# Performance work log

Measured on AMD Instinct MI355X. Metric: run time of the kernel, lower is better.

Reference implementation:

```python
import jax, jax.numpy as jnp
import numpy as np

N = 50000
E = 800000
IN_CH = 128
HID = 64
HEADS = 4
EPS = 1e-5
NEG_SLOPE = 0.2


def _gat_conv(x, src, dst, W, a_src, a_dst, b, heads, out_ch, concat):
    n = x.shape[0]
    h = (x @ W).reshape(n, heads, out_ch)                      # [N,H,C]
    alpha_src = jnp.sum(h * a_src, axis=-1)                    # [N,H]
    alpha_dst = jnp.sum(h * a_dst, axis=-1)                    # [N,H]
    e = jax.nn.leaky_relu(alpha_src[src] + alpha_dst[dst], NEG_SLOPE)  # [E',H]
    # segment softmax over incoming edges of each destination node
    m = jax.ops.segment_max(e, dst, num_segments=n)            # [N,H]
    e = jnp.exp(e - m[dst])
    denom = jax.ops.segment_sum(e, dst, num_segments=n)        # [N,H]
    alpha = e / denom[dst]                                     # [E',H]
    msg = h[src] * alpha[:, :, None]                           # [E',H,C]
    out = jax.ops.segment_sum(msg, dst, num_segments=n)        # [N,H,C]
    if concat:
        out = out.reshape(n, heads * out_ch)
    else:
        out = out.mean(axis=1)
    return out + b


def _bn_eval(x, gamma, beta, mean, var):
    return (x - mean) * (gamma / jnp.sqrt(var + EPS)) + beta


def setup_inputs() -> dict:
    key = jax.random.key(0)
    ks = jax.random.split(key, 24)
    s = 0.1
    x = jax.random.normal(ks[0], (N, IN_CH), dtype=jnp.float32)
    edge_index = jax.random.randint(ks[1], (2, E), 0, N, dtype=jnp.int32)
    d0, d1 = IN_CH, HID * HEADS
    inp = {
        'x': x, 'edge_index': edge_index,
        # layer 0: in_ch -> hidden, heads=4, concat
        'W0': jax.random.normal(ks[2], (d0, HEADS * HID), jnp.float32) * s,
        'as0': jax.random.normal(ks[3], (HEADS, HID), jnp.float32) * s,
        'ad0': jax.random.normal(ks[4], (HEADS, HID), jnp.float32) * s,
        'b0': jax.random.normal(ks[5], (HEADS * HID,), jnp.float32) * s,
        # layer 1: hidden*heads -> hidden, heads=4, concat
        'W1': jax.random.normal(ks[6], (d1, HEADS * HID), jnp.float32) * s,
        'as1': jax.random.normal(ks[7], (HEADS, HID), jnp.float32) * s,
        'ad1': jax.random.normal(ks[8], (HEADS, HID), jnp.float32) * s,
        'b1': jax.random.normal(ks[9], (HEADS * HID,), jnp.float32) * s,
        # layer 2: hidden*heads -> 1, heads=1, no concat
        'W2': jax.random.normal(ks[10], (d1, 1), jnp.float32) * s,
        'as2': jax.random.normal(ks[11], (1, 1), jnp.float32) * s,
        'ad2': jax.random.normal(ks[12], (1, 1), jnp.float32) * s,
        'b2': jax.random.normal(ks[13], (1,), jnp.float32) * s,
        # batchnorm (eval) params for the two hidden layers
        'g0': jnp.ones((d1,), jnp.float32),
        'be0': jnp.zeros((d1,), jnp.float32),
        'm0': jax.random.normal(ks[14], (d1,), jnp.float32) * s,
        'v0': jnp.ones((d1,), jnp.float32),
        'g1': jnp.ones((d1,), jnp.float32),
        'be1': jnp.zeros((d1,), jnp.float32),
        'm1': jax.random.normal(ks[15], (d1,), jnp.float32) * s,
        'v1': jnp.ones((d1,), jnp.float32),
    }
    return inp


def reference(x, edge_index, W0, as0, ad0, b0, W1, as1, ad1, b1,
              W2, as2, ad2, b2, g0, be0, m0, v0, g1, be1, m1, v1):
    n = x.shape[0]
    loops = jnp.arange(n, dtype=edge_index.dtype)
    src = jnp.concatenate([edge_index[0], loops])  # add self-loops (PyG default)
    dst = jnp.concatenate([edge_index[1], loops])

    # layer 0 (no residual: shapes differ)
    h = _gat_conv(x, src, dst, W0, as0, ad0, b0, HEADS, HID, True)
    h = jax.nn.elu(_bn_eval(h, g0, be0, m0, v0))

    # layer 1 (residual: shapes match)
    res = h
    h = _gat_conv(h, src, dst, W1, as1, ad1, b1, HEADS, HID, True)
    h = jax.nn.elu(_bn_eval(h, g1, be1, m1, v1)) + res

    # output layer: heads=1, concat=False -> [N,1]
    out = _gat_conv(h, src, dst, W2, as2, ad2, b2, 1, 1, False)
    return out.squeeze(-1)
```

## Files before the change

kernel.cpp:

```cpp
#include <hip/hip_runtime.h>
#include <math.h>

#define NEG_SLOPE 0.2f
#define BN_EPS 1e-5f

typedef __attribute__((ext_vector_type(8))) short bf16x8;
typedef __attribute__((ext_vector_type(4))) float f32x4;

static __device__ __forceinline__ unsigned short f2bf(float f){
    unsigned u = __float_as_uint(f);
    u += 0x7FFFu + ((u >> 16) & 1u);
    return (unsigned short)(u >> 16);
}
static __device__ __forceinline__ float bf2f(unsigned short v){
    return __uint_as_float((unsigned)v << 16);
}

static __device__ __forceinline__ void gload_lds16(const void* g, void* l){
    __builtin_amdgcn_global_load_lds(
        (const __attribute__((address_space(1))) void*)g,
        (__attribute__((address_space(3))) void*)l, 16, 0, 0);
}

static __device__ __forceinline__ void repack_one(const float* __restrict__ W,
    unsigned short* __restrict__ whi, unsigned short* __restrict__ wlo, int o)
{
    const int j = o & 7, ln = (o >> 3) & 63, ct = (o >> 9) & 15, kt = o >> 13;
    const int k = kt * 32 + 8 * (ln >> 4) + j;
    const int col = ct * 16 + (ln & 15);
    const float v = W[k * 256 + col];
    const unsigned short hb = f2bf(v);
    whi[o] = hb; wlo[o] = f2bf(v - bf2f(hb));
}

__global__ void prep_kernel(const float* __restrict__ W0,
    unsigned short* __restrict__ w0hi, unsigned short* __restrict__ w0lo,
    const float* __restrict__ W1,
    unsigned short* __restrict__ w1hi, unsigned short* __restrict__ w1lo,
    int* __restrict__ deg, int N)
{
    const int bid = blockIdx.x, t = threadIdx.x;
    if (bid < 128){
        repack_one(W0, w0hi, w0lo, bid * 256 + t);
    } else if (bid < 384){
        repack_one(W1, w1hi, w1lo, (bid - 128) * 256 + t);
    } else {
        const int i = (bid - 384) * 256 + t;
        if (i < N) deg[i] = 1;
    }
}

template<int K>
__global__ __launch_bounds__(256) void mfma_gemm_alpha(
    const float* __restrict__ x,
    const unsigned short* __restrict__ wbhi, const unsigned short* __restrict__ wblo,
    const float* __restrict__ a_s, const float* __restrict__ a_d,
    unsigned short* __restrict__ hout,
    float* __restrict__ asrc, float* __restrict__ adst, int N)
{
    __shared__ float xaf[4][2][64][4];
    __shared__ unsigned short wb[32][512];
    const int t = threadIdx.x, lane = t & 63, wid = t >> 6;
    const int n0 = blockIdx.x * 64;

    f32x4 acc[4][4];
#pragma unroll
    for (int rt = 0; rt < 4; ++rt)
#pragma unroll
        for (int q = 0; q < 4; ++q) acc[rt][q] = (f32x4){0.f, 0.f, 0.f, 0.f};

    for (int kt = 0; kt < K / 32; ++kt){
        __syncthreads();
#pragma unroll
        for (int ii = 0; ii < 2; ++ii){
            const int i = wid * 2 + ii;
            const int rt = i >> 1, half = i & 1;
            int node = n0 + rt * 16 + (lane & 15);
            if (node > N - 1) node = N - 1;
            const float* src = &x[(size_t)node * K + kt * 32 + 8 * (lane >> 4) + half * 4];
            gload_lds16(src, &xaf[rt][half][0][0]);
        }
#pragma unroll
        for (int ii = 0; ii < 8; ++ii){
            const int i = wid * 8 + ii;
            const int ct = i >> 1, plane = i & 1;
            const unsigned short* base = plane ? wblo : wbhi;
            gload_lds16(base + ((size_t)(kt * 16 + ct) * 64 + lane) * 8, &wb[i][0]);
        }
        __syncthreads();

        bf16x8 ahi[4], alo[4];
#pragma unroll
        for (int rt = 0; rt < 4; ++rt){
            const float4 f0 = *(const float4*)&xaf[rt][0][lane][0];
            const float4 f1 = *(const float4*)&xaf[rt][1][lane][0];
            const float fv[8] = {f0.x, f0.y, f0.z, f0.w, f1.x, f1.y, f1.z, f1.w};
#pragma unroll
            for (int j = 0; j < 8; ++j){
                const unsigned short hb = f2bf(fv[j]);
                ahi[rt][j] = (short)hb;
                alo[rt][j] = (short)f2bf(fv[j] - bf2f(hb));
            }
        }

#pragma unroll
        for (int q = 0; q < 4; ++q){
            const int cti = wid * 4 + q;
            const bf16x8 bhi = *(const bf16x8*)&wb[cti * 2 + 0][lane * 8];
            const bf16x8 blo = *(const bf16x8*)&wb[cti * 2 + 1][lane * 8];
#pragma unroll
            for (int rt = 0; rt < 4; ++rt){
                acc[rt][q] = __builtin_amdgcn_mfma_f32_16x16x32_bf16(ahi[rt], bhi, acc[rt][q], 0, 0, 0);
                acc[rt][q] = __builtin_amdgcn_mfma_f32_16x16x32_bf16(alo[rt], bhi, acc[rt][q], 0, 0, 0);
                acc[rt][q] = __builtin_amdgcn_mfma_f32_16x16x32_bf16(ahi[rt], blo, acc[rt][q], 0, 0, 0);
            }
        }
    }

    const int l15 = lane & 15, lg = lane >> 4;
    float avs[4], avd[4];
#pragma unroll
    for (int q = 0; q < 4; ++q){
        avs[q] = a_s[wid * 64 + q * 16 + l15];
        avd[q] = a_d[wid * 64 + q * 16 + l15];
    }
    float sp[4][4], dp[4][4];
#pragma unroll
    for (int rt = 0; rt < 4; ++rt){
#pragma unroll
        for (int reg = 0; reg < 4; ++reg){
            const int node = n0 + rt * 16 + lg * 4 + reg;
            float s = 0.f, d = 0.f;
            unsigned short hv[4];
#pragma unroll
            for (int q = 0; q < 4; ++q){
                const float v = acc[rt][q][reg];
                s = fmaf(v, avs[q], s); d = fmaf(v, avd[q], d);
                hv[q] = f2bf(v);
            }
            if (node < N){
#pragma unroll
                for (int q = 0; q < 4; ++q)
                    hout[(size_t)node * 256 + (wid * 4 + q) * 16 + l15] = hv[q];
            }
            sp[rt][reg] = s; dp[rt][reg] = d;
        }
    }
#pragma unroll
    for (int off = 1; off <= 8; off <<= 1){
#pragma unroll
        for (int rt = 0; rt < 4; ++rt)
#pragma unroll
            for (int reg = 0; reg < 4; ++reg){
                sp[rt][reg] += __shfl_xor(sp[rt][reg], off, 64);
                dp[rt][reg] += __shfl_xor(dp[rt][reg], off, 64);
            }
    }
    if (l15 == 0){
#pragma unroll
        for (int rt = 0; rt < 4; ++rt)
#pragma unroll
            for (int reg = 0; reg < 4; ++reg){
                const int node = n0 + rt * 16 + lg * 4 + reg;
                if (node < N){
                    asrc[(size_t)node * 4 + wid] = sp[rt][reg];
                    adst[(size_t)node * 4 + wid] = dp[rt][reg];
                }
            }
    }
}

__global__ void deg_hist_kernel(const int* __restrict__ ei, int E, int* __restrict__ deg){
    int e = blockIdx.x * blockDim.x + threadIdx.x;
    if (e < E) atomicAdd(&deg[ei[E + e]], 1);
}

__global__ __launch_bounds__(256) void part_sum_kernel(const int* __restrict__ deg,
                                                       int* __restrict__ bsum, int N)
{
    __shared__ int red[256];
    const int t = threadIdx.x;
    const int i0 = blockIdx.x * 1024 + t * 4;
    int s = 0;
    if (i0 + 3 < N){
        const int4 v = *(const int4*)&deg[i0];
        s = v.x + v.y + v.z + v.w;
    } else {
#pragma unroll
        for (int j = 0; j < 4; ++j) if (i0 + j < N) s += deg[i0 + j];
    }
    red[t] = s; __syncthreads();
    for (int off = 128; off >= 1; off >>= 1){
        if (t < off) red[t] += red[t + off];
        __syncthreads();
    }
    if (t == 0) bsum[blockIdx.x] = red[0];
}

__global__ __launch_bounds__(256) void scan_part_kernel(int* __restrict__ bsum, int nb,
                                                        int* __restrict__ row, int N)
{
    __shared__ int sh[256];
    const int t = threadIdx.x;
    const int v = (t < nb) ? bsum[t] : 0;
    sh[t] = v; __syncthreads();
    for (int off = 1; off < 256; off <<= 1){
        int u = (t >= off) ? sh[t - off] : 0;
        __syncthreads();
        sh[t] += u;
        __syncthreads();
    }
    if (t < nb) bsum[t] = sh[t] - v;
    if (t == nb - 1) row[N] = sh[t];
}

__global__ __launch_bounds__(256) void distribute_kernel(const int* __restrict__ deg,
    const int* __restrict__ bsum, int* __restrict__ row, int* __restrict__ cursor, int N)
{
    __shared__ int ts[256];
    const int t = threadIdx.x;
    const int i0 = blockIdx.x * 1024 + t * 4;
    int d[4]; int s = 0;
#pragma unroll
    for (int j = 0; j < 4; ++j){ d[j] = (i0 + j < N) ? deg[i0 + j] : 0; s += d[j]; }
    ts[t] = s; __syncthreads();
    for (int off = 1; off < 256; off <<= 1){
        int u = (t >= off) ? ts[t - off] : 0;
        __syncthreads();
        ts[t] += u;
        __syncthreads();
    }
    int base = bsum[blockIdx.x] + ts[t] - s;
#pragma unroll
    for (int j = 0; j < 4; ++j){
        if (i0 + j < N){ row[i0 + j] = base; cursor[i0 + j] = base; base += d[j]; }
    }
}

__global__ void scatter_kernel(const int* __restrict__ ei, int E, int N,
                               int* __restrict__ cursor, int* __restrict__ csr)
{
    int e = blockIdx.x * blockDim.x + threadIdx.x;
    if (e >= E + N) return;
    int s, d;
    if (e < E){ s = ei[e]; d = ei[E + e]; } else { s = d = e - E; }
    int pos = atomicAdd(&cursor[d], 1);
    csr[pos] = s;
}

#define DEG_CAP 128
template<bool LAST>
__global__ __launch_bounds__(256) void agg4_kernel(
    const int* __restrict__ row, const int* __restrict__ csr,
    const float* __restrict__ asrc, const float* __restrict__ adst,
    const unsigned short* __restrict__ h,
    const float* __restrict__ b, const float* __restrict__ g,
    const float* __restrict__ be, const float* __restrict__ mean,
    const float* __restrict__ var,
    const float* __restrict__ res,
    float* __restrict__ outp,
    const float* __restrict__ W2,
    int N)
{
    __shared__ float plds[4][DEG_CAP * 4];
    __shared__ int   slds[4][DEG_CAP];
    const int wid = threadIdx.x >> 6, lane = threadIdx.x & 63;
    const int node = blockIdx.x * 4 + wid;
    if (node >= N) return;
    const int beg = row[node], end = row[node + 1], deg = end - beg;
    const int degc = deg < DEG_CAP ? deg : DEG_CAP;
    const int head = lane >> 4;

    const float4 ad = *(const float4*)&adst[(size_t)node * 4];

    float d0 = 0.f, d1 = 0.f, d2 = 0.f, d3 = 0.f;
    for (int i = lane; i < deg; i += 64){
        const int s = csr[beg + i];
        const float4 as = *(const float4*)&asrc[(size_t)s * 4];
        float v0 = as.x + ad.x, v1 = as.y + ad.y, v2 = as.z + ad.z, v3 = as.w + ad.w;
        v0 = v0 > 0.f ? v0 : NEG_SLOPE * v0;
        v1 = v1 > 0.f ? v1 : NEG_SLOPE * v1;
        v2 = v2 > 0.f ? v2 : NEG_SLOPE * v2;
        v3 = v3 > 0.f ? v3 : NEG_SLOPE * v3;
        const float p0 = __expf(v0), p1 = __expf(v1);
        const float p2 = __expf(v2), p3 = __expf(v3);
        d0 += p0; d1 += p1; d2 += p2; d3 += p3;
        if (i < DEG_CAP){
            *(float4*)&plds[wid][i * 4] = make_float4(p0, p1, p2, p3);
            slds[wid][i] = s << 9;
        }
    }
    for (int off = 32; off >= 1; off >>= 1){
        d0 += __shfl_xor(d0, off, 64); d1 += __shfl_xor(d1, off, 64);
        d2 += __shfl_xor(d2, off, 64); d3 += __shfl_xor(d3, off, 64);
    }

    float a0 = 0.f, a1 = 0.f, a2 = 0.f, a3 = 0.f;
    {
        const char* hb = (const char*)h + lane * 8;
        const float* pb = &plds[wid][0];
        const int* sb = &slds[wid][0];
#define EDGE_BODY(slot)                                                        \
        {                                                                      \
            const float p_ = pb[(slot) * 4 + head];                            \
            const ushort4 hv_ = *(const ushort4*)(hb + sb[slot]);              \
            a0 = fmaf(p_, bf2f(hv_.x), a0); a1 = fmaf(p_, bf2f(hv_.y), a1);    \
            a2 = fmaf(p_, bf2f(hv_.z), a2); a3 = fmaf(p_, bf2f(hv_.w), a3);    \
        }
        int i = 0;
        for (; i + 2 <= degc; i += 2){
            EDGE_BODY(i);
            EDGE_BODY(i + 1);
        }
        for (; i < degc; ++i) EDGE_BODY(i);
#undef EDGE_BODY
    }

    for (int jj = beg + DEG_CAP; jj < end; ++jj){
        const int s = csr[jj];
        const float4 as = *(const float4*)&asrc[(size_t)s * 4];
        float e0 = as.x + ad.x, e1 = as.y + ad.y, e2 = as.z + ad.z, e3 = as.w + ad.w;
        float eh = (head == 0) ? e0 : (head == 1) ? e1 : (head == 2) ? e2 : e3;
        eh = eh > 0.f ? eh : NEG_SLOPE * eh;
        const float p = __expf(eh);
        const ushort4 hv = *(const ushort4*)&h[(size_t)s * 256 + lane * 4];
        a0 = fmaf(p, bf2f(hv.x), a0); a1 = fmaf(p, bf2f(hv.y), a1);
        a2 = fmaf(p, bf2f(hv.z), a2); a3 = fmaf(p, bf2f(hv.w), a3);
    }

    const int l15 = lane & 15;
    const float dsel = (head == 0) ? d0 : (head == 1) ? d1 : (head == 2) ? d2 : d3;
    const float rdi = 1.f / dsel;
    const int c0 = head * 64 + 4 * l15;
    const float4 bv  = *(const float4*)&b[c0];
    const float4 gv  = *(const float4*)&g[c0];
    const float4 bev = *(const float4*)&be[c0];
    const float4 mv  = *(const float4*)&mean[c0];
    const float4 vv4 = *(const float4*)&var[c0];
    const float ava[4]  = {a0, a1, a2, a3};
    const float bva[4]  = {bv.x, bv.y, bv.z, bv.w};
    const float gva[4]  = {gv.x, gv.y, gv.z, gv.w};
    const float beva[4] = {bev.x, bev.y, bev.z, bev.w};
    const float mva[4]  = {mv.x, mv.y, mv.z, mv.w};
    const float vva[4]  = {vv4.x, vv4.y, vv4.z, vv4.w};
    float rh[4] = {0.f, 0.f, 0.f, 0.f};
    if (LAST){
        const float4 rv = *(const float4*)&res[(size_t)node * 256 + c0];
        rh[0] = rv.x; rh[1] = rv.y; rh[2] = rv.z; rh[3] = rv.w;
    }
    float vvv[4];
#pragma unroll
    for (int j = 0; j < 4; ++j){
        float v = ava[j] * rdi + bva[j];
        v = (v - mva[j]) * (gva[j] * rsqrtf(vva[j] + BN_EPS)) + beva[j];
        v = v > 0.f ? v : (__expf(v) - 1.f);
        vvv[j] = v + rh[j];
    }
    if (!LAST){
        *(float4*)&outp[(size_t)node * 256 + c0] =
            make_float4(vvv[0], vvv[1], vvv[2], vvv[3]);
    } else {
        const float4 w2v = *(const float4*)&W2[c0];
        float part = vvv[0] * w2v.x + vvv[1] * w2v.y + vvv[2] * w2v.z + vvv[3] * w2v.w;
        for (int off = 32; off >= 1; off >>= 1) part += __shfl_xor(part, off, 64);
        if (lane == 0) outp[node] = part;
    }
}

__global__ void agg2_kernel(const int* __restrict__ row, const int* __restrict__ csr,
                            const float* __restrict__ h2,
                            const float* __restrict__ as2, const float* __restrict__ ad2,
                            const float* __restrict__ b2, float* __restrict__ out, int N)
{
    const int n = blockIdx.x * blockDim.x + threadIdx.x;
    if (n >= N) return;
    const float A_s = as2[0];
    const float hd  = h2[n] * ad2[0];
    const int beg = row[n], end = row[n + 1];
    float den = 0.f, acc = 0.f;
    for (int i = beg; i < end; ++i){
        const float hv = h2[csr[i]];
        float a = fmaf(A_s, hv, hd);
        a = a > 0.f ? a : NEG_SLOPE * a;
        const float p = __expf(a);
        den += p; acc = fmaf(p, hv, acc);
    }
    out[n] = acc / den + b2[0];
}

extern "C" void kernel_launch(void* const* d_in, const int* in_sizes, int n_in,
                              void* d_out, int out_size, void* d_ws, size_t ws_size,
                              hipStream_t stream)
{
    const float* x   = (const float*)d_in[0];
    const int*   ei  = (const int*)  d_in[1];
    const float* W0  = (const float*)d_in[2];
    const float* as0 = (const float*)d_in[3];
    const float* ad0 = (const float*)d_in[4];
    const float* b0  = (const float*)d_in[5];
    const float* W1  = (const float*)d_in[6];
    const float* as1 = (const float*)d_in[7];
    const float* ad1 = (const float*)d_in[8];
    const float* b1  = (const float*)d_in[9];
    const float* W2  = (const float*)d_in[10];
    const float* as2 = (const float*)d_in[11];
    const float* ad2 = (const float*)d_in[12];
    const float* b2  = (const float*)d_in[13];
    const float* g0  = (const float*)d_in[14];
    const float* be0 = (const float*)d_in[15];
    const float* m0  = (const float*)d_in[16];
    const float* v0  = (const float*)d_in[17];
    const float* g1  = (const float*)d_in[18];
    const float* be1 = (const float*)d_in[19];
    const float* m1  = (const float*)d_in[20];
    const float* v1  = (const float*)d_in[21];

    const int N = in_sizes[0] / 128;
    const int E = in_sizes[1] / 2;
    const int EN = E + N;

    char* w = (char*)d_ws;
    unsigned short* H  = (unsigned short*)w;  w += (size_t)N * 256 * 2;
    float*    P0     = (float*)w;   w += (size_t)N * 256 * 4;
    float*    asrc   = (float*)w;   w += (size_t)N * 4 * 4;
    float*    adst   = (float*)w;   w += (size_t)N * 4 * 4;
    int*      deg    = (int*)w;     w += (size_t)N * 4;
    int*      cursor = (int*)w;     w += (size_t)N * 4;
    int*      csr    = (int*)w;     w += (size_t)EN * 4;
    float*    h2     = (float*)w;   w += (size_t)N * 4;
    int*      bsum   = (int*)w;     w += 1024;
    unsigned short* Wb0hi = (unsigned short*)w; w += (size_t)128 * 256 * 2;
    unsigned short* Wb0lo = (unsigned short*)w; w += (size_t)128 * 256 * 2;
    unsigned short* Wb1hi = (unsigned short*)w; w += (size_t)256 * 256 * 2;
    unsigned short* Wb1lo = (unsigned short*)w; w += (size_t)256 * 256 * 2;
    int*      rowp   = (int*)w;     w += (size_t)(N + 1) * 4;

    const int gN64  = (N + 63) / 64;
    const int gN4   = (N + 3) / 4;
    const int gNt   = (N + 255) / 256;
    const int gE    = (E + 255) / 256;
    const int gEN   = (EN + 255) / 256;
    const int nb    = (N + 1023) / 1024;

    prep_kernel<<<384 + gNt, 256, 0, stream>>>(W0, Wb0hi, Wb0lo, W1, Wb1hi, Wb1lo, deg, N);
    deg_hist_kernel<<<gE, 256, 0, stream>>>(ei, E, deg);
    part_sum_kernel<<<nb, 256, 0, stream>>>(deg, bsum, N);
    scan_part_kernel<<<1, 256, 0, stream>>>(bsum, nb, rowp, N);
    distribute_kernel<<<nb, 256, 0, stream>>>(deg, bsum, rowp, cursor, N);
    scatter_kernel<<<gEN, 256, 0, stream>>>(ei, E, N, cursor, csr);

    mfma_gemm_alpha<128><<<gN64, 256, 0, stream>>>(x, Wb0hi, Wb0lo,
                                                   as0, ad0, H, asrc, adst, N);
    agg4_kernel<false><<<gN4, 256, 0, stream>>>(rowp, csr, asrc, adst, H,
                                                b0, g0, be0, m0, v0,
                                                nullptr, P0, nullptr, N);

    mfma_gemm_alpha<256><<<gN64, 256, 0, stream>>>(P0, Wb1hi, Wb1lo,
                                                   as1, ad1, H, asrc, adst, N);
    agg4_kernel<true><<<gN4, 256, 0, stream>>>(rowp, csr, asrc, adst, H,
                                               b1, g1, be1, m1, v1,
                                               P0, h2, W2, N);

    agg2_kernel<<<gNt, 256, 0, stream>>>(rowp, csr, h2, as2, ad2, b2, (float*)d_out, N);
}
```

Baseline: 331.5 us.

## Store layer-0 activations in bf16 and specialize layer-1 GEMM for bf16 input

The layer-0 aggregation output (also the residual) is now written as bf16 instead of fp32. A dedicated layer-1 GEMM loads the bf16 activations straight into LDS and drops the hi/lo split of A, going from three MFMAs per tile to two. The gather loop in the aggregation is also unrolled by 8 so more loads are in flight. This cuts activation traffic and MFMA work, but loses precision in the layer-1 input and in the residual.

```diff
diff --git a/kernel.cpp b/kernel.cpp
--- a/kernel.cpp
+++ b/kernel.cpp
@@ -50,14 +50,14 @@
     }
 }
 
-template<int K>
-__global__ __launch_bounds__(256) void mfma_gemm_alpha(
+__global__ __launch_bounds__(256) void mfma_gemm0(
     const float* __restrict__ x,
     const unsigned short* __restrict__ wbhi, const unsigned short* __restrict__ wblo,
     const float* __restrict__ a_s, const float* __restrict__ a_d,
     unsigned short* __restrict__ hout,
     float* __restrict__ asrc, float* __restrict__ adst, int N)
 {
+    constexpr int K = 128;
     __shared__ float xaf[4][2][64][4];
     __shared__ unsigned short wb[32][512];
     const int t = threadIdx.x, lane = t & 63, wid = t >> 6;
@@ -113,6 +113,114 @@
                 acc[rt][q] = __builtin_amdgcn_mfma_f32_16x16x32_bf16(ahi[rt], bhi, acc[rt][q], 0, 0, 0);
                 acc[rt][q] = __builtin_amdgcn_mfma_f32_16x16x32_bf16(alo[rt], bhi, acc[rt][q], 0, 0, 0);
                 acc[rt][q] = __builtin_amdgcn_mfma_f32_16x16x32_bf16(ahi[rt], blo, acc[rt][q], 0, 0, 0);
+            }
+        }
+    }
+
+    const int l15 = lane & 15, lg = lane >> 4;
+    float avs[4], avd[4];
+#pragma unroll
+    for (int q = 0; q < 4; ++q){
+        avs[q] = a_s[wid * 64 + q * 16 + l15];
+        avd[q] = a_d[wid * 64 + q * 16 + l15];
+    }
+    float sp[4][4], dp[4][4];
+#pragma unroll
+    for (int rt = 0; rt < 4; ++rt){
+#pragma unroll
+        for (int reg = 0; reg < 4; ++reg){
+            const int node = n0 + rt * 16 + lg * 4 + reg;
+            float s = 0.f, d = 0.f;
+            unsigned short hv[4];
+#pragma unroll
+            for (int q = 0; q < 4; ++q){
+                const float v = acc[rt][q][reg];
+                s = fmaf(v, avs[q], s); d = fmaf(v, avd[q], d);
+                hv[q] = f2bf(v);
+            }
+            if (node < N){
+#pragma unroll
+                for (int q = 0; q < 4; ++q)
+                    hout[(size_t)node * 256 + (wid * 4 + q) * 16 + l15] = hv[q];
+            }
+            sp[rt][reg] = s; dp[rt][reg] = d;
+        }
+    }
+#pragma unroll
+    for (int off = 1; off <= 8; off <<= 1){
+#pragma unroll
+        for (int rt = 0; rt < 4; ++rt)
+#pragma unroll
+            for (int reg = 0; reg < 4; ++reg){
+                sp[rt][reg] += __shfl_xor(sp[rt][reg], off, 64);
+                dp[rt][reg] += __shfl_xor(dp[rt][reg], off, 64);
+            }
+    }
+    if (l15 == 0){
+#pragma unroll
+        for (int rt = 0; rt < 4; ++rt)
+#pragma unroll
+            for (int reg = 0; reg < 4; ++reg){
+                const int node = n0 + rt * 16 + lg * 4 + reg;
+                if (node < N){
+                    asrc[(size_t)node * 4 + wid] = sp[rt][reg];
+                    adst[(size_t)node * 4 + wid] = dp[rt][reg];
+                }
+            }
+    }
+}
+
+__global__ __launch_bounds__(256) void mfma_gemm1(
+    const unsigned short* __restrict__ xb,
+    const unsigned short* __restrict__ wbhi, const unsigned short* __restrict__ wblo,
+    const float* __restrict__ a_s, const float* __restrict__ a_d,
+    unsigned short* __restrict__ hout,
+    float* __restrict__ asrc, float* __restrict__ adst, int N)
+{
+    constexpr int K = 256;
+    __shared__ unsigned short xab[4][512];
+    __shared__ unsigned short wb[32][512];
+    const int t = threadIdx.x, lane = t & 63, wid = t >> 6;
+    const int n0 = blockIdx.x * 64;
+
+    f32x4 acc[4][4];
+#pragma unroll
+    for (int rt = 0; rt < 4; ++rt)
+#pragma unroll
+        for (int q = 0; q < 4; ++q) acc[rt][q] = (f32x4){0.f, 0.f, 0.f, 0.f};
+
+    for (int kt = 0; kt < K / 32; ++kt){
+        __syncthreads();
+        {
+            const int rt = wid;
+            int node = n0 + rt * 16 + (lane & 15);
+            if (node > N - 1) node = N - 1;
+            const unsigned short* src = &xb[(size_t)node * K + kt * 32 + 8 * (lane >> 4)];
+            gload_lds16(src, &xab[rt][0]);
+        }
+#pragma unroll
+        for (int ii = 0; ii < 8; ++ii){
+            const int i = wid * 8 + ii;
+            const int ct = i >> 1, plane = i & 1;
+            const unsigned short* base = plane ? wblo : wbhi;
+            gload_lds16(base + ((size_t)(kt * 16 + ct) * 64 + lane) * 8, &wb[i][0]);
+        }
+        __syncthreads();
+
+        bf16x8 a[4];
+#pragma unroll
+        for (int rt = 0; rt < 4; ++rt)
+            a[rt] = *(const bf16x8*)&xab[rt][lane * 8];
+
+#pragma unroll
+        for (int q = 0; q < 4; ++q){
+            const int cti = wid * 4 + q;
+            const bf16x8 bhi = *(const bf16x8*)&wb[cti * 2 + 0][lane * 8];
+            const bf16x8 blo = *(const bf16x8*)&wb[cti * 2 + 1][lane * 8];
+#pragma unroll
+            for (int rt = 0; rt < 4; ++rt){
+                acc[rt][q] = __builtin_amdgcn_mfma_f32_16x16x32_bf16(a[rt], bhi, acc[rt][q], 0, 0, 0);
+                acc[rt][q] = __builtin_amdgcn_mfma_f32_16x16x32_bf16(a[rt], blo, acc[rt][q], 0, 0, 0);
             }
         }
     }
@@ -257,8 +365,9 @@
     const float* __restrict__ b, const float* __restrict__ g,
     const float* __restrict__ be, const float* __restrict__ mean,
     const float* __restrict__ var,
-    const float* __restrict__ res,
-    float* __restrict__ outp,
+    const unsigned short* __restrict__ res,
+    unsigned short* __restrict__ outbf,
+    float* __restrict__ outh2,
     const float* __restrict__ W2,
     int N)
 {
@@ -300,20 +409,24 @@
         const char* hb = (const char*)h + lane * 8;
         const float* pb = &plds[wid][0];
         const int* sb = &slds[wid][0];
-#define EDGE_BODY(slot)                                                        \
-        {                                                                      \
-            const float p_ = pb[(slot) * 4 + head];                            \
-            const ushort4 hv_ = *(const ushort4*)(hb + sb[slot]);              \
-            a0 = fmaf(p_, bf2f(hv_.x), a0); a1 = fmaf(p_, bf2f(hv_.y), a1);    \
-            a2 = fmaf(p_, bf2f(hv_.z), a2); a3 = fmaf(p_, bf2f(hv_.w), a3);    \
-        }
         int i = 0;
-        for (; i + 2 <= degc; i += 2){
-            EDGE_BODY(i);
-            EDGE_BODY(i + 1);
-        }
-        for (; i < degc; ++i) EDGE_BODY(i);
-#undef EDGE_BODY
+        for (; i + 8 <= degc; i += 8){
+            ushort4 hv[8];
+#pragma unroll
+            for (int u = 0; u < 8; ++u) hv[u] = *(const ushort4*)(hb + sb[i + u]);
+#pragma unroll
+            for (int u = 0; u < 8; ++u){
+                const float p_ = pb[(i + u) * 4 + head];
+                a0 = fmaf(p_, bf2f(hv[u].x), a0); a1 = fmaf(p_, bf2f(hv[u].y), a1);
+                a2 = fmaf(p_, bf2f(hv[u].z), a2); a3 = fmaf(p_, bf2f(hv[u].w), a3);
+            }
+        }
+        for (; i < degc; ++i){
+            const float p_ = pb[i * 4 + head];
+            const ushort4 hv_ = *(const ushort4*)(hb + sb[i]);
+            a0 = fmaf(p_, bf2f(hv_.x), a0); a1 = fmaf(p_, bf2f(hv_.y), a1);
+            a2 = fmaf(p_, bf2f(hv_.z), a2); a3 = fmaf(p_, bf2f(hv_.w), a3);
+        }
     }
 
     for (int jj = beg + DEG_CAP; jj < end; ++jj){
@@ -345,8 +458,8 @@
     const float vva[4]  = {vv4.x, vv4.y, vv4.z, vv4.w};
     float rh[4] = {0.f, 0.f, 0.f, 0.f};
     if (LAST){
-        const float4 rv = *(const float4*)&res[(size_t)node * 256 + c0];
-        rh[0] = rv.x; rh[1] = rv.y; rh[2] = rv.z; rh[3] = rv.w;
+        const ushort4 rv = *(const ushort4*)&res[(size_t)node * 256 + c0];
+        rh[0] = bf2f(rv.x); rh[1] = bf2f(rv.y); rh[2] = bf2f(rv.z); rh[3] = bf2f(rv.w);
     }
     float vvv[4];
 #pragma unroll
@@ -357,13 +470,15 @@
         vvv[j] = v + rh[j];
     }
     if (!LAST){
-        *(float4*)&outp[(size_t)node * 256 + c0] =
-            make_float4(vvv[0], vvv[1], vvv[2], vvv[3]);
+        ushort4 o4;
+        o4.x = f2bf(vvv[0]); o4.y = f2bf(vvv[1]);
+        o4.z = f2bf(vvv[2]); o4.w = f2bf(vvv[3]);
+        *(ushort4*)&outbf[(size_t)node * 256 + c0] = o4;
     } else {
         const float4 w2v = *(const float4*)&W2[c0];
         float part = vvv[0] * w2v.x + vvv[1] * w2v.y + vvv[2] * w2v.z + vvv[3] * w2v.w;
         for (int off = 32; off >= 1; off >>= 1) part += __shfl_xor(part, off, 64);
-        if (lane == 0) outp[node] = part;
+        if (lane == 0) outh2[node] = part;
     }
 }
 
@@ -420,8 +535,8 @@
     const int EN = E + N;
 
     char* w = (char*)d_ws;
-    unsigned short* H  = (unsigned short*)w;  w += (size_t)N * 256 * 2;
-    float*    P0     = (float*)w;   w += (size_t)N * 256 * 4;
+    unsigned short* H    = (unsigned short*)w;  w += (size_t)N * 256 * 2;
+    unsigned short* P0   = (unsigned short*)w;  w += (size_t)N * 256 * 2;
     float*    asrc   = (float*)w;   w += (size_t)N * 4 * 4;
     float*    adst   = (float*)w;   w += (size_t)N * 4 * 4;
     int*      deg    = (int*)w;     w += (size_t)N * 4;
@@ -449,17 +564,17 @@
     distribute_kernel<<<nb, 256, 0, stream>>>(deg, bsum, rowp, cursor, N);
     scatter_kernel<<<gEN, 256, 0, stream>>>(ei, E, N, cursor, csr);
 
-    mfma_gemm_alpha<128><<<gN64, 256, 0, stream>>>(x, Wb0hi, Wb0lo,
-                                                   as0, ad0, H, asrc, adst, N);
+    mfma_gemm0<<<gN64, 256, 0, stream>>>(x, Wb0hi, Wb0lo,
+                                         as0, ad0, H, asrc, adst, N);
     agg4_kernel<false><<<gN4, 256, 0, stream>>>(rowp, csr, asrc, adst, H,
                                                 b0, g0, be0, m0, v0,
-                                                nullptr, P0, nullptr, N);
-
-    mfma_gemm_alpha<256><<<gN64, 256, 0, stream>>>(P0, Wb1hi, Wb1lo,
-                                                   as1, ad1, H, asrc, adst, N);
+                                                nullptr, P0, nullptr, nullptr, N);
+
+    mfma_gemm1<<<gN64, 256, 0, stream>>>(P0, Wb1hi, Wb1lo,
+                                         as1, ad1, H, asrc, adst, N);
     agg4_kernel<true><<<gN4, 256, 0, stream>>>(rowp, csr, asrc, adst, H,
                                                b1, g1, be1, m1, v1,
-                                               P0, h2, W2, N);
+                                               P0, nullptr, h2, W2, N);
 
     agg2_kernel<<<gNt, 256, 0, stream>>>(rowp, csr, h2, as2, ad2, b2, (float*)d_out, N);
 }
```

Measured after the change: 321.1 us. 1.03x faster.
